# Performance work log

Measured on AMD Instinct MI355X. Metric: run time of the kernel, lower is better.

## Reference

```python
import jax, jax.numpy as jnp
import numpy as np

UNITS = 1024
N_FEATURES = 128
OUT_STEPS = 32
EPS = 1e-7


def _lstm_cell(x, h, c, W, U, b):
    # Keras LSTMCell: gates ordered i, f, g(candidate), o
    z = x @ W + h @ U + b  # [B, 4U]
    i, f, g, o = jnp.split(z, 4, axis=-1)
    i = jax.nn.sigmoid(i)
    f = jax.nn.sigmoid(f)
    g = jnp.tanh(g)
    o = jax.nn.sigmoid(o)
    c_new = f * c + i * g
    h_new = o * jnp.tanh(c_new)
    return h_new, c_new


def setup_inputs() -> dict:
    key = jax.random.key(0)
    ks = jax.random.split(key, 12)
    B, T, F, U = 512, 64, N_FEATURES, UNITS
    s = lambda fan_in: 1.0 / np.sqrt(fan_in)
    return {
        "inputs": jax.random.normal(ks[0], (B, T, F), jnp.float32),
        "mean": jax.random.normal(ks[1], (F,), jnp.float32) * 0.1,
        "var": jax.random.uniform(ks[2], (F,), jnp.float32, 0.5, 1.5),
        "W1": jax.random.normal(ks[3], (F, 4 * U), jnp.float32) * s(F),
        "U1": jax.random.normal(ks[4], (U, 4 * U), jnp.float32) * s(U),
        "b1": jnp.zeros((4 * U,), jnp.float32),
        "W2": jax.random.normal(ks[5], (U, 4 * U), jnp.float32) * s(U),
        "U2": jax.random.normal(ks[6], (U, 4 * U), jnp.float32) * s(U),
        "b2": jnp.zeros((4 * U,), jnp.float32),
        "Wd": jax.random.normal(ks[7], (U, F), jnp.float32) * s(U),
        "bd": jnp.zeros((F,), jnp.float32),
    }


def reference(inputs, mean, var, W1, U1, b1, W2, U2, b2, Wd, bd):
    B = inputs.shape[0]
    inv_std = jax.lax.rsqrt(var + EPS)
    # NOTE: original call() normalizes, then warmup() normalizes AGAIN -- faithful.
    x = (inputs - mean) * inv_std
    x = (x - mean) * inv_std

    # --- warmup: RNN(cell1) over input sequence, return last h and state ---
    h0 = jnp.zeros((B, UNITS), x.dtype)
    c0 = jnp.zeros((B, UNITS), x.dtype)

    def warm_step(carry, xt):
        h, c = carry
        h, c = _lstm_cell(xt, h, c, W1, U1, b1)
        return (h, c), None

    (h, c), _ = jax.lax.scan(warm_step, (h0, c0), jnp.swapaxes(x, 0, 1))
    pred0 = h @ Wd + bd  # [B, F]

    def ar_step(carry, _):
        pred, h, c = carry
        h, c = _lstm_cell(pred, h, c, W1, U1, b1)
        h, c = _lstm_cell(h, h, c, W2, U2, b2)
        pred = h @ Wd + bd
        return (pred, h, c), pred

    _, preds = jax.lax.scan(ar_step, (pred0, h, c), None, length=OUT_STEPS - 1)
    preds = jnp.concatenate([pred0[None], preds], axis=0)  # [out_steps, B, F]
    return jnp.transpose(preds, (1, 0, 2))  # [B, out_steps, F]
```

## Files before the change

### kernel.cpp

```cpp
#include <hip/hip_runtime.h>
#include <stdint.h>

#define NB 512
#define NT 64
#define NF 128
#define NU 1024
#define NG 4096
#define NS 32

typedef __attribute__((ext_vector_type(8))) short short8;
typedef __attribute__((ext_vector_type(4))) float f32x4;
typedef __attribute__((ext_vector_type(4))) unsigned int u32x4;

__device__ __forceinline__ float sigm(float x) { return 1.0f / (1.0f + __expf(-x)); }
__device__ __forceinline__ float tanh_f(float x) {
  float ax = fabsf(x);
  float e = __expf(2.0f * ax);
  float t = 1.0f - 2.0f / (e + 1.0f);
  return copysignf(t, x);
}
__device__ __forceinline__ unsigned short f2bf(float f) {
  union { float f; unsigned u; } v; v.f = f;
  unsigned r = v.u + 0x7fffu + ((v.u >> 16) & 1u);
  return (unsigned short)(r >> 16);
}

__device__ __forceinline__ void coh_store_bf16(unsigned short* p, unsigned v) {
  asm volatile("global_store_short %0, %1, off sc0 sc1" :: "v"(p), "v"(v) : "memory");
}

__device__ __forceinline__ void gbar(unsigned* flags, int bid, unsigned gen) {
  __syncthreads();
  if (threadIdx.x == 0)
    __hip_atomic_store(flags + bid, gen, __ATOMIC_RELAXED, __HIP_MEMORY_SCOPE_AGENT);
  if (bid == 0) {
    if (threadIdx.x < 256) {
      while (__hip_atomic_load(flags + threadIdx.x, __ATOMIC_RELAXED, __HIP_MEMORY_SCOPE_AGENT) != gen)
        __builtin_amdgcn_s_sleep(1);
    }
    __syncthreads();
    if (threadIdx.x == 0)
      __hip_atomic_store(flags + 256, gen, __ATOMIC_RELAXED, __HIP_MEMORY_SCOPE_AGENT);
  } else if (threadIdx.x == 0) {
    while (__hip_atomic_load(flags + 256, __ATOMIC_RELAXED, __HIP_MEMORY_SCOPE_AGENT) != gen)
      __builtin_amdgcn_s_sleep(1);
  }
  __syncthreads();
}

template <int KX>
__device__ __forceinline__ void do_step(
    const unsigned short* __restrict__ hIn,
    const unsigned short* __restrict__ Bp,
    const unsigned short* __restrict__ Xp,
    const unsigned short* __restrict__ W1p,
    int tstep, f32x4 bA, f32x4 (&cst)[2],
    unsigned short* __restrict__ hOut, unsigned short* __restrict__ hOut2,
    unsigned short* lds,
    int r0, int u0, int kh, int wu, int lr, int g4, int ucol, int tid)
{
  constexpr int ROWE = NU + KX;

  {
    u32x4 t[8];
    const unsigned short* src[8];
    int loff[8];
#pragma unroll
    for (int it = 0; it < 8; ++it) {
      int i = tid + it * 512;
      int r = i >> 7, cb = i & 127;
      src[it] = hIn + (size_t)(r0 + r) * NU + cb * 8;
      loff[it] = r * (ROWE * 2) + ((cb * 16) ^ ((r & 7) << 4));
    }
#pragma unroll
    for (int it = 0; it < 8; ++it)
      asm volatile("global_load_dwordx4 %0, %1, off sc0 sc1" : "=v"(t[it]) : "v"(src[it]));
    if constexpr (KX > 0) {
      int r = tid >> 4, cb = tid & 15;
      u32x4 vx = *(const u32x4*)(Xp + ((size_t)tstep * NB + (r0 + r)) * NF + cb * 8);
      int ox = r * (ROWE * 2) + ((NU * 2 + cb * 16) ^ ((r & 7) << 4));
      asm volatile("s_waitcnt vmcnt(0)" ::: "memory");
      __builtin_amdgcn_sched_barrier(0);
#pragma unroll
      for (int it = 0; it < 8; ++it) *(u32x4*)((char*)lds + loff[it]) = t[it];
      *(u32x4*)((char*)lds + ox) = vx;
    } else {
      asm volatile("s_waitcnt vmcnt(0)" ::: "memory");
      __builtin_amdgcn_sched_barrier(0);
#pragma unroll
      for (int it = 0; it < 8; ++it) *(u32x4*)((char*)lds + loff[it]) = t[it];
    }
  }
  __syncthreads();

  f32x4 acc[4][2];
#pragma unroll
  for (int g = 0; g < 4; ++g)
#pragma unroll
    for (int rt = 0; rt < 2; ++rt) acc[g][rt] = (f32x4){0.f, 0.f, 0.f, 0.f};

  const char* ldsb = (const char*)lds;
  const int arow0 = lr * (ROWE * 2);
  const int arow1 = (16 + lr) * (ROWE * 2);
  const int axor = (lr & 7) << 4;
  const int kcb = kh * 16;

  short8 nb[2][4];
  {
    size_t b0 = ((size_t)(kcb * 4 + g4) * NG + ucol) * 8;
    size_t b1 = ((size_t)((kcb + 1) * 4 + g4) * NG + ucol) * 8;
#pragma unroll
    for (int g = 0; g < 4; ++g) {
      nb[0][g] = *(const short8*)(Bp + b0 + (size_t)g * NU * 8);
      nb[1][g] = *(const short8*)(Bp + b1 + (size_t)g * NU * 8);
    }
  }
#pragma unroll 4
  for (int kc = 0; kc < 16; ++kc) {
    short8 bb[4];
#pragma unroll
    for (int g = 0; g < 4; ++g) bb[g] = nb[kc & 1][g];
    if (kc < 14) {
      size_t base = ((size_t)((kcb + kc + 2) * 4 + g4) * NG + ucol) * 8;
#pragma unroll
      for (int g = 0; g < 4; ++g) nb[kc & 1][g] = *(const short8*)(Bp + base + (size_t)g * NU * 8);
    }
    int kb = ((kcb + kc) * 64 + g4 * 16) ^ axor;
    short8 a0 = *(const short8*)(ldsb + arow0 + kb);
    short8 a1 = *(const short8*)(ldsb + arow1 + kb);
#pragma unroll
    for (int g = 0; g < 4; ++g) {
      acc[g][0] = __builtin_amdgcn_mfma_f32_16x16x32_bf16(a0, bb[g], acc[g][0], 0, 0, 0);
      acc[g][1] = __builtin_amdgcn_mfma_f32_16x16x32_bf16(a1, bb[g], acc[g][1], 0, 0, 0);
    }
  }
  if constexpr (KX > 0) {
#pragma unroll
    for (int kc = kh * 2; kc < kh * 2 + 2; ++kc) {
      int kb = (NU * 2 + kc * 64 + g4 * 16) ^ axor;
      short8 a0 = *(const short8*)(ldsb + arow0 + kb);
      short8 a1 = *(const short8*)(ldsb + arow1 + kb);
      size_t base = ((size_t)(kc * 4 + g4) * NG + ucol) * 8;
      short8 bb[4];
#pragma unroll
      for (int g = 0; g < 4; ++g) bb[g] = *(const short8*)(W1p + base + (size_t)g * NU * 8);
#pragma unroll
      for (int g = 0; g < 4; ++g) {
        acc[g][0] = __builtin_amdgcn_mfma_f32_16x16x32_bf16(a0, bb[g], acc[g][0], 0, 0, 0);
        acc[g][1] = __builtin_amdgcn_mfma_f32_16x16x32_bf16(a1, bb[g], acc[g][1], 0, 0, 0);
      }
    }
  }

  __syncthreads();
  float* red = (float*)lds;
  const int l = (g4 << 4) | lr;
  if (kh == 1) {
#pragma unroll
    for (int g = 0; g < 4; ++g)
#pragma unroll
      for (int rt = 0; rt < 2; ++rt)
        *(f32x4*)(red + (size_t)(((wu * 8) + (g * 2 + rt)) * 64 + l) * 4) = acc[g][rt];
  }
  __syncthreads();
  if (kh == 0) {
#pragma unroll
    for (int g = 0; g < 4; ++g)
#pragma unroll
      for (int rt = 0; rt < 2; ++rt)
        acc[g][rt] += *(const f32x4*)(red + (size_t)(((wu * 8) + (g * 2 + rt)) * 64 + l) * 4);

#pragma unroll
    for (int rt = 0; rt < 2; ++rt) {
#pragma unroll
      for (int j = 0; j < 4; ++j) {
        int r = r0 + rt * 16 + g4 * 4 + j;
        size_t idx = (size_t)r * NU + ucol;
        float iv = sigm(acc[0][rt][j] + bA[0]);
        float fv = sigm(acc[1][rt][j] + bA[1]);
        float gv = tanh_f(acc[2][rt][j] + bA[2]);
        float ov = sigm(acc[3][rt][j] + bA[3]);
        float cN = fv * cst[rt][j] + iv * gv;
        cst[rt][j] = cN;
        unsigned hv = f2bf(ov * tanh_f(cN));
        coh_store_bf16(hOut + idx, hv);
        if (hOut2) coh_store_bf16(hOut2 + idx, hv);
      }
    }
  }
}

__global__ __launch_bounds__(512, 2) void lstm_seq(
    const unsigned short* __restrict__ U1p, const unsigned short* __restrict__ U1pp,
    const unsigned short* __restrict__ W2U2p, const unsigned short* __restrict__ W1p,
    const unsigned short* __restrict__ x2,
    const float* __restrict__ b1, const float* __restrict__ b1p, const float* __restrict__ b2,
    unsigned short* __restrict__ h0, unsigned short* __restrict__ h1,
    unsigned short* __restrict__ hist, unsigned* __restrict__ flags)
{
  extern __shared__ unsigned short lds[];
  const int bid = blockIdx.x;
  const int xcd = bid & 7, slot = bid >> 3;
  const int u_blk = xcd * 2 + (slot >> 4);
  const int m_blk = slot & 15;
  const int r0 = m_blk * 32, u0 = u_blk * 64;
  const int tid = threadIdx.x;
  const int w = tid >> 6, kh = w >> 2, wu = w & 3;
  const int lr = tid & 15, g4 = (tid >> 4) & 3;
  const int ucol = u0 + wu * 16 + lr;
  const size_t HS = (size_t)NB * NU;

  f32x4 bW, bC1, bC2;
#pragma unroll
  for (int g = 0; g < 4; ++g) {
    bW[g]  = b1 [g * NU + ucol];
    bC1[g] = b1p[g * NU + ucol];
    bC2[g] = b2 [g * NU + ucol];
  }
  f32x4 cst[2];
  cst[0] = (f32x4){0.f, 0.f, 0.f, 0.f};
  cst[1] = (f32x4){0.f, 0.f, 0.f, 0.f};

  unsigned gen = 0;
  for (int t = 0; t < NT; ++t) {
    const unsigned short* hi = (t & 1) ? h1 : h0;
    unsigned short* ho = (t & 1) ? h0 : h1;
    do_step<NF>(hi, U1p, x2, W1p, t, bW, cst, ho, (t == NT - 1) ? hist : nullptr,
                lds, r0, u0, kh, wu, lr, g4, ucol, tid);
    gbar(flags, bid, ++gen);
  }
  for (int s = 0; s < NS - 1; ++s) {
    do_step<0>(h0, U1pp, nullptr, nullptr, 0, bC1, cst, h1, nullptr,
               lds, r0, u0, kh, wu, lr, g4, ucol, tid);
    gbar(flags, bid, ++gen);
    do_step<0>(h1, W2U2p, nullptr, nullptr, 0, bC2, cst, h0, hist + (size_t)(s + 1) * HS,
               lds, r0, u0, kh, wu, lr, g4, ucol, tid);
    if (s < NS - 2) gbar(flags, bid, ++gen);
  }
}

__global__ __launch_bounds__(256, 2) void pred_gemm(
    const unsigned short* __restrict__ H,
    const unsigned short* __restrict__ Wdp,
    const float* __restrict__ bd, float* __restrict__ out)
{
  __shared__ unsigned short lds[32 * NU];
  const int tid = threadIdx.x;
  const int r0 = blockIdx.x * 32;
  for (int i = tid; i < 32 * 128; i += 256) {
    int r = i >> 7, cb = i & 127;
    uint4 v = *(const uint4*)(H + (size_t)(r0 + r) * NU + cb * 8);
    int off = r * 2048 + ((cb * 16) ^ ((r & 7) << 4));
    *(uint4*)((char*)lds + off) = v;
  }
  __syncthreads();
  const int w = tid >> 6, l = tid & 63, lr = l & 15, g4 = l >> 4;
  f32x4 acc[2][2];
#pragma unroll
  for (int a = 0; a < 2; ++a)
#pragma unroll
    for (int c = 0; c < 2; ++c) acc[a][c] = (f32x4){0.f, 0.f, 0.f, 0.f};
  const char* ldsb = (const char*)lds;
  const int arow0 = lr * 2048, arow1 = (16 + lr) * 2048, axor = (lr & 7) << 4;
  const int col0 = w * 32 + lr;
#pragma unroll 4
  for (int kc = 0; kc < 32; ++kc) {
    int kb = (kc * 64 + g4 * 16) ^ axor;
    short8 a0 = *(const short8*)(ldsb + arow0 + kb);
    short8 a1 = *(const short8*)(ldsb + arow1 + kb);
    size_t base = ((size_t)(kc * 4 + g4) * NF) * 8;
    short8 w0 = *(const short8*)(Wdp + base + (size_t)col0 * 8);
    short8 w1 = *(const short8*)(Wdp + base + (size_t)(col0 + 16) * 8);
    acc[0][0] = __builtin_amdgcn_mfma_f32_16x16x32_bf16(a0, w0, acc[0][0], 0, 0, 0);
    acc[1][0] = __builtin_amdgcn_mfma_f32_16x16x32_bf16(a1, w0, acc[1][0], 0, 0, 0);
    acc[0][1] = __builtin_amdgcn_mfma_f32_16x16x32_bf16(a0, w1, acc[0][1], 0, 0, 0);
    acc[1][1] = __builtin_amdgcn_mfma_f32_16x16x32_bf16(a1, w1, acc[1][1], 0, 0, 0);
  }
#pragma unroll
  for (int rt = 0; rt < 2; ++rt)
#pragma unroll
    for (int ct = 0; ct < 2; ++ct)
#pragma unroll
      for (int j = 0; j < 4; ++j) {
        int r = r0 + rt * 16 + g4 * 4 + j;
        int s = r >> 9, bb = r & 511;
        int f = w * 32 + ct * 16 + lr;
        out[((size_t)bb * NS + s) * NF + f] = acc[rt][ct][j] + bd[f];
      }
}

__global__ void prep_x(const float* __restrict__ in, const float* __restrict__ mean,
                       const float* __restrict__ var, unsigned short* __restrict__ x2) {
  int i = (blockIdx.x * 256 + threadIdx.x) * 4;
  int f = i & 127;
  int bt = i >> 7;
  int b = bt >> 6, t = bt & 63;
  float4 v = *(const float4*)(in + i);
  float vv[4] = {v.x, v.y, v.z, v.w};
  unsigned short o[4] __attribute__((aligned(8)));
#pragma unroll
  for (int j = 0; j < 4; ++j) {
    float inv = rsqrtf(var[f + j] + 1e-7f);
    float s = inv * inv;
    float m2 = mean[f + j] * (s + inv);
    o[j] = f2bf(vv[j] * s - m2);
  }
  *(uint2*)(x2 + (((size_t)t * NB + b) << 7) + f) = *(const uint2*)o;
}

__global__ void prep_pack(const float* __restrict__ A, const float* __restrict__ A2,
                          unsigned short* __restrict__ P, int N) {
  int idx = blockIdx.x * 256 + threadIdx.x;
  int kg = idx / N, c = idx - kg * N;
  unsigned short o[8] __attribute__((aligned(16)));
#pragma unroll
  for (int j = 0; j < 8; ++j) {
    size_t e = (size_t)(kg * 8 + j) * N + c;
    float vv = A[e];
    if (A2) vv += A2[e];
    o[j] = f2bf(vv);
  }
  *(uint4*)(P + (size_t)idx * 8) = *(const uint4*)o;
}

__global__ __launch_bounds__(256) void prep_u1pp(
    const float* __restrict__ U1, const float* __restrict__ Wd,
    const float* __restrict__ W1, unsigned short* __restrict__ P) {
  __shared__ float wd[8][NF];
  const int kg = blockIdx.x >> 4;
  const int c = ((blockIdx.x & 15) << 8) + threadIdx.x;
  for (int i = threadIdx.x; i < 8 * NF; i += 256)
    wd[i >> 7][i & 127] = Wd[(size_t)(kg * 8 + (i >> 7)) * NF + (i & 127)];
  __syncthreads();
  float a[8];
#pragma unroll
  for (int j = 0; j < 8; ++j) a[j] = U1[(size_t)(kg * 8 + j) * NG + c];
#pragma unroll 8
  for (int m = 0; m < NF; ++m) {
    float w1v = W1[(size_t)m * NG + c];
#pragma unroll
    for (int j = 0; j < 8; ++j) a[j] += wd[j][m] * w1v;
  }
  unsigned short o[8] __attribute__((aligned(16)));
#pragma unroll
  for (int j = 0; j < 8; ++j) o[j] = f2bf(a[j]);
  *(uint4*)(P + (size_t)(kg * NG + c) * 8) = *(const uint4*)o;
}

__global__ void prep_wdp(const float* __restrict__ Wd, unsigned short* __restrict__ P) {
  int idx = blockIdx.x * 256 + threadIdx.x;
  int kg = idx >> 7, f = idx & 127;
  unsigned short o[8] __attribute__((aligned(16)));
#pragma unroll
  for (int j = 0; j < 8; ++j) o[j] = f2bf(Wd[(size_t)(kg * 8 + j) * NF + f]);
  *(uint4*)(P + (size_t)idx * 8) = *(const uint4*)o;
}

__global__ void prep_b1p(const float* __restrict__ b1, const float* __restrict__ bd,
                         const float* __restrict__ W1, float* __restrict__ o) {
  int c = blockIdx.x * 256 + threadIdx.x;
  float acc = b1[c];
#pragma unroll 8
  for (int m = 0; m < NF; ++m) acc += bd[m] * W1[(size_t)m * NG + c];
  o[c] = acc;
}

extern "C" void kernel_launch(void* const* d_in, const int* in_sizes, int n_in,
                              void* d_out, int out_size, void* d_ws, size_t ws_size,
                              hipStream_t stream) {
  const float* inputs = (const float*)d_in[0];
  const float* mean = (const float*)d_in[1];
  const float* var  = (const float*)d_in[2];
  const float* W1   = (const float*)d_in[3];
  const float* U1   = (const float*)d_in[4];
  const float* b1   = (const float*)d_in[5];
  const float* W2   = (const float*)d_in[6];
  const float* U2   = (const float*)d_in[7];
  const float* b2   = (const float*)d_in[8];
  const float* Wd   = (const float*)d_in[9];
  const float* bd   = (const float*)d_in[10];
  float* out = (float*)d_out;
  char* ws = (char*)d_ws;

  size_t off = 0;
  auto alloc = [&](size_t bytes) { char* p = ws + off; off += (bytes + 255) & ~255ull; return p; };
  unsigned short* h0    = (unsigned short*)alloc((size_t)NB * NU * 2);
  unsigned short* h1    = (unsigned short*)alloc((size_t)NB * NU * 2);
  unsigned short* hist  = (unsigned short*)alloc((size_t)NS * NB * NU * 2);
  unsigned short* x2    = (unsigned short*)alloc((size_t)NB * NT * NF * 2);
  unsigned short* U1p   = (unsigned short*)alloc((size_t)NU * NG * 2);
  unsigned short* U1pp  = (unsigned short*)alloc((size_t)NU * NG * 2);
  unsigned short* W2U2p = (unsigned short*)alloc((size_t)NU * NG * 2);
  unsigned short* W1p   = (unsigned short*)alloc((size_t)NF * NG * 2);
  unsigned short* Wdp   = (unsigned short*)alloc((size_t)NU * NF * 2);
  float* b1p            = (float*)alloc((size_t)NG * 4);
  unsigned* flags       = (unsigned*)alloc(2048);

  hipMemsetAsync(h0, 0, (size_t)NB * NU * 2, stream);
  hipMemsetAsync(flags, 0, 2048, stream);

  prep_x   <<<(NB * NT * NF) / 1024, 256, 0, stream>>>(inputs, mean, var, x2);
  prep_pack<<<(NU / 8) * NG / 256, 256, 0, stream>>>(U1, nullptr, U1p, NG);
  prep_u1pp<<<(NU / 8) * NG / 256, 256, 0, stream>>>(U1, Wd, W1, U1pp);
  prep_pack<<<(NU / 8) * NG / 256, 256, 0, stream>>>(W2, U2, W2U2p, NG);
  prep_pack<<<(NF / 8) * NG / 256, 256, 0, stream>>>(W1, nullptr, W1p, NG);
  prep_wdp <<<(NU / 8) * NF / 256, 256, 0, stream>>>(Wd, Wdp);
  prep_b1p <<<NG / 256, 256, 0, stream>>>(b1, bd, W1, b1p);

  lstm_seq<<<256, 512, 98304, stream>>>(U1p, U1pp, W2U2p, W1p, x2,
                                        b1, b1p, b2, h0, h1, hist, flags);

  pred_gemm<<<(NS * NB) / 32, 256, 0, stream>>>(hist, Wdp, bd, out);
}
```

Before: 1.353 ms.

## Retile persistent LSTM blocks to 64x32 with 4-way K split

```diff
diff --git a/kernel.cpp b/kernel.cpp
--- a/kernel.cpp
+++ b/kernel.cpp
@@ -25,14 +25,10 @@
   return (unsigned short)(r >> 16);
 }
 
-__device__ __forceinline__ void coh_store_bf16(unsigned short* p, unsigned v) {
-  asm volatile("global_store_short %0, %1, off sc0 sc1" :: "v"(p), "v"(v) : "memory");
-}
-
 __device__ __forceinline__ void gbar(unsigned* flags, int bid, unsigned gen) {
   __syncthreads();
   if (threadIdx.x == 0)
-    __hip_atomic_store(flags + bid, gen, __ATOMIC_RELAXED, __HIP_MEMORY_SCOPE_AGENT);
+    __hip_atomic_store(flags + bid, gen, __ATOMIC_RELEASE, __HIP_MEMORY_SCOPE_AGENT);
   if (bid == 0) {
     if (threadIdx.x < 256) {
       while (__hip_atomic_load(flags + threadIdx.x, __ATOMIC_RELAXED, __HIP_MEMORY_SCOPE_AGENT) != gen)
@@ -54,124 +50,131 @@
     const unsigned short* __restrict__ Bp,
     const unsigned short* __restrict__ Xp,
     const unsigned short* __restrict__ W1p,
-    int tstep, f32x4 bA, f32x4 (&cst)[2],
+    int tstep, f32x4 bA, f32x4 (&cst)[4],
     unsigned short* __restrict__ hOut, unsigned short* __restrict__ hOut2,
     unsigned short* lds,
     int r0, int u0, int kh, int wu, int lr, int g4, int ucol, int tid)
 {
-  constexpr int ROWE = NU + KX;
+  constexpr int ROWB = (NU + KX) * 2;
 
   {
-    u32x4 t[8];
-    const unsigned short* src[8];
-    int loff[8];
-#pragma unroll
-    for (int it = 0; it < 8; ++it) {
+    u32x4 t[16];
+    const unsigned short* src[16];
+    int loff[16];
+#pragma unroll
+    for (int it = 0; it < 16; ++it) {
       int i = tid + it * 512;
       int r = i >> 7, cb = i & 127;
       src[it] = hIn + (size_t)(r0 + r) * NU + cb * 8;
-      loff[it] = r * (ROWE * 2) + ((cb * 16) ^ ((r & 7) << 4));
-    }
-#pragma unroll
-    for (int it = 0; it < 8; ++it)
+      loff[it] = r * ROWB + ((cb * 16) ^ ((r & 7) << 4));
+    }
+#pragma unroll
+    for (int it = 0; it < 16; ++it)
       asm volatile("global_load_dwordx4 %0, %1, off sc0 sc1" : "=v"(t[it]) : "v"(src[it]));
     if constexpr (KX > 0) {
-      int r = tid >> 4, cb = tid & 15;
-      u32x4 vx = *(const u32x4*)(Xp + ((size_t)tstep * NB + (r0 + r)) * NF + cb * 8);
-      int ox = r * (ROWE * 2) + ((NU * 2 + cb * 16) ^ ((r & 7) << 4));
+      u32x4 vx[2]; int ox[2];
+#pragma unroll
+      for (int it = 0; it < 2; ++it) {
+        int i = tid + it * 512;
+        int r = i >> 4, cb = i & 15;
+        vx[it] = *(const u32x4*)(Xp + ((size_t)tstep * NB + (r0 + r)) * NF + cb * 8);
+        ox[it] = r * ROWB + ((NU * 2 + cb * 16) ^ ((r & 7) << 4));
+      }
       asm volatile("s_waitcnt vmcnt(0)" ::: "memory");
       __builtin_amdgcn_sched_barrier(0);
 #pragma unroll
-      for (int it = 0; it < 8; ++it) *(u32x4*)((char*)lds + loff[it]) = t[it];
-      *(u32x4*)((char*)lds + ox) = vx;
+      for (int it = 0; it < 16; ++it) *(u32x4*)((char*)lds + loff[it]) = t[it];
+#pragma unroll
+      for (int it = 0; it < 2; ++it) *(u32x4*)((char*)lds + ox[it]) = vx[it];
     } else {
       asm volatile("s_waitcnt vmcnt(0)" ::: "memory");
       __builtin_amdgcn_sched_barrier(0);
 #pragma unroll
-      for (int it = 0; it < 8; ++it) *(u32x4*)((char*)lds + loff[it]) = t[it];
-    }
-  }
-  __syncthreads();
-
-  f32x4 acc[4][2];
+      for (int it = 0; it < 16; ++it) *(u32x4*)((char*)lds + loff[it]) = t[it];
+    }
+  }
+  __syncthreads();
+
+  f32x4 acc[4][4];
 #pragma unroll
   for (int g = 0; g < 4; ++g)
 #pragma unroll
-    for (int rt = 0; rt < 2; ++rt) acc[g][rt] = (f32x4){0.f, 0.f, 0.f, 0.f};
+    for (int rt = 0; rt < 4; ++rt) acc[g][rt] = (f32x4){0.f, 0.f, 0.f, 0.f};
 
   const char* ldsb = (const char*)lds;
-  const int arow0 = lr * (ROWE * 2);
-  const int arow1 = (16 + lr) * (ROWE * 2);
+  int arow[4];
+#pragma unroll
+  for (int rt = 0; rt < 4; ++rt) arow[rt] = (rt * 16 + lr) * ROWB;
   const int axor = (lr & 7) << 4;
-  const int kcb = kh * 16;
+  const int kcb = kh * 8;
 
   short8 nb[2][4];
-  {
-    size_t b0 = ((size_t)(kcb * 4 + g4) * NG + ucol) * 8;
-    size_t b1 = ((size_t)((kcb + 1) * 4 + g4) * NG + ucol) * 8;
-#pragma unroll
-    for (int g = 0; g < 4; ++g) {
-      nb[0][g] = *(const short8*)(Bp + b0 + (size_t)g * NU * 8);
-      nb[1][g] = *(const short8*)(Bp + b1 + (size_t)g * NU * 8);
-    }
-  }
-#pragma unroll 4
-  for (int kc = 0; kc < 16; ++kc) {
+#pragma unroll
+  for (int p = 0; p < 2; ++p) {
+    size_t base = ((size_t)((kcb + p) * 4 + g4) * NG + ucol) * 8;
+#pragma unroll
+    for (int g = 0; g < 4; ++g) nb[p][g] = *(const short8*)(Bp + base + (size_t)g * NU * 8);
+  }
+#pragma unroll
+  for (int kc = 0; kc < 8; ++kc) {
     short8 bb[4];
 #pragma unroll
     for (int g = 0; g < 4; ++g) bb[g] = nb[kc & 1][g];
-    if (kc < 14) {
+    if (kc < 6) {
       size_t base = ((size_t)((kcb + kc + 2) * 4 + g4) * NG + ucol) * 8;
 #pragma unroll
       for (int g = 0; g < 4; ++g) nb[kc & 1][g] = *(const short8*)(Bp + base + (size_t)g * NU * 8);
     }
     int kb = ((kcb + kc) * 64 + g4 * 16) ^ axor;
-    short8 a0 = *(const short8*)(ldsb + arow0 + kb);
-    short8 a1 = *(const short8*)(ldsb + arow1 + kb);
-#pragma unroll
-    for (int g = 0; g < 4; ++g) {
-      acc[g][0] = __builtin_amdgcn_mfma_f32_16x16x32_bf16(a0, bb[g], acc[g][0], 0, 0, 0);
-      acc[g][1] = __builtin_amdgcn_mfma_f32_16x16x32_bf16(a1, bb[g], acc[g][1], 0, 0, 0);
-    }
+    short8 a[4];
+#pragma unroll
+    for (int rt = 0; rt < 4; ++rt) a[rt] = *(const short8*)(ldsb + arow[rt] + kb);
+#pragma unroll
+    for (int g = 0; g < 4; ++g)
+#pragma unroll
+      for (int rt = 0; rt < 4; ++rt)
+        acc[g][rt] = __builtin_amdgcn_mfma_f32_16x16x32_bf16(a[rt], bb[g], acc[g][rt], 0, 0, 0);
   }
   if constexpr (KX > 0) {
-#pragma unroll
-    for (int kc = kh * 2; kc < kh * 2 + 2; ++kc) {
-      int kb = (NU * 2 + kc * 64 + g4 * 16) ^ axor;
-      short8 a0 = *(const short8*)(ldsb + arow0 + kb);
-      short8 a1 = *(const short8*)(ldsb + arow1 + kb);
-      size_t base = ((size_t)(kc * 4 + g4) * NG + ucol) * 8;
-      short8 bb[4];
-#pragma unroll
-      for (int g = 0; g < 4; ++g) bb[g] = *(const short8*)(W1p + base + (size_t)g * NU * 8);
-#pragma unroll
-      for (int g = 0; g < 4; ++g) {
-        acc[g][0] = __builtin_amdgcn_mfma_f32_16x16x32_bf16(a0, bb[g], acc[g][0], 0, 0, 0);
-        acc[g][1] = __builtin_amdgcn_mfma_f32_16x16x32_bf16(a1, bb[g], acc[g][1], 0, 0, 0);
-      }
-    }
-  }
-
-  __syncthreads();
+    int kb = (NU * 2 + kh * 64 + g4 * 16) ^ axor;
+    size_t base = ((size_t)(kh * 4 + g4) * NG + ucol) * 8;
+    short8 bb[4];
+#pragma unroll
+    for (int g = 0; g < 4; ++g) bb[g] = *(const short8*)(W1p + base + (size_t)g * NU * 8);
+    short8 a[4];
+#pragma unroll
+    for (int rt = 0; rt < 4; ++rt) a[rt] = *(const short8*)(ldsb + arow[rt] + kb);
+#pragma unroll
+    for (int g = 0; g < 4; ++g)
+#pragma unroll
+      for (int rt = 0; rt < 4; ++rt)
+        acc[g][rt] = __builtin_amdgcn_mfma_f32_16x16x32_bf16(a[rt], bb[g], acc[g][rt], 0, 0, 0);
+  }
+
+  __syncthreads();
+  const int l = (g4 << 4) | lr;
   float* red = (float*)lds;
-  const int l = (g4 << 4) | lr;
-  if (kh == 1) {
+  if (kh != 0) {
+    float* base = red + (size_t)((kh - 1) * 2 + wu) * 4096;
 #pragma unroll
     for (int g = 0; g < 4; ++g)
 #pragma unroll
-      for (int rt = 0; rt < 2; ++rt)
-        *(f32x4*)(red + (size_t)(((wu * 8) + (g * 2 + rt)) * 64 + l) * 4) = acc[g][rt];
+      for (int rt = 0; rt < 4; ++rt)
+        *(f32x4*)(base + ((g * 4 + rt) * 64 + l) * 4) = acc[g][rt];
   }
   __syncthreads();
   if (kh == 0) {
 #pragma unroll
-    for (int g = 0; g < 4; ++g)
-#pragma unroll
-      for (int rt = 0; rt < 2; ++rt)
-        acc[g][rt] += *(const f32x4*)(red + (size_t)(((wu * 8) + (g * 2 + rt)) * 64 + l) * 4);
-
-#pragma unroll
-    for (int rt = 0; rt < 2; ++rt) {
+    for (int s = 0; s < 3; ++s) {
+      float* base = red + (size_t)(s * 2 + wu) * 4096;
+#pragma unroll
+      for (int g = 0; g < 4; ++g)
+#pragma unroll
+        for (int rt = 0; rt < 4; ++rt)
+          acc[g][rt] += *(const f32x4*)(base + ((g * 4 + rt) * 64 + l) * 4);
+    }
+#pragma unroll
+    for (int rt = 0; rt < 4; ++rt) {
 #pragma unroll
       for (int j = 0; j < 4; ++j) {
         int r = r0 + rt * 16 + g4 * 4 + j;
@@ -182,15 +185,15 @@
         float ov = sigm(acc[3][rt][j] + bA[3]);
         float cN = fv * cst[rt][j] + iv * gv;
         cst[rt][j] = cN;
-        unsigned hv = f2bf(ov * tanh_f(cN));
-        coh_store_bf16(hOut + idx, hv);
-        if (hOut2) coh_store_bf16(hOut2 + idx, hv);
+        unsigned short hv = f2bf(ov * tanh_f(cN));
+        hOut[idx] = hv;
+        if (hOut2) hOut2[idx] = hv;
       }
     }
   }
 }
 
-__global__ __launch_bounds__(512, 2) void lstm_seq(
+__global__ __launch_bounds__(512, 1) void lstm_seq(
     const unsigned short* __restrict__ U1p, const unsigned short* __restrict__ U1pp,
     const unsigned short* __restrict__ W2U2p, const unsigned short* __restrict__ W1p,
     const unsigned short* __restrict__ x2,
@@ -201,11 +204,11 @@
   extern __shared__ unsigned short lds[];
   const int bid = blockIdx.x;
   const int xcd = bid & 7, slot = bid >> 3;
-  const int u_blk = xcd * 2 + (slot >> 4);
-  const int m_blk = slot & 15;
-  const int r0 = m_blk * 32, u0 = u_blk * 64;
+  const int u_blk = xcd * 4 + (slot >> 3);
+  const int m_blk = slot & 7;
+  const int r0 = m_blk * 64, u0 = u_blk * 32;
   const int tid = threadIdx.x;
-  const int w = tid >> 6, kh = w >> 2, wu = w & 3;
+  const int w = tid >> 6, kh = w >> 1, wu = w & 1;
   const int lr = tid & 15, g4 = (tid >> 4) & 3;
   const int ucol = u0 + wu * 16 + lr;
   const size_t HS = (size_t)NB * NU;
@@ -217,9 +220,9 @@
     bC1[g] = b1p[g * NU + ucol];
     bC2[g] = b2 [g * NU + ucol];
   }
-  f32x4 cst[2];
-  cst[0] = (f32x4){0.f, 0.f, 0.f, 0.f};
-  cst[1] = (f32x4){0.f, 0.f, 0.f, 0.f};
+  f32x4 cst[4];
+#pragma unroll
+  for (int rt = 0; rt < 4; ++rt) cst[rt] = (f32x4){0.f, 0.f, 0.f, 0.f};
 
   unsigned gen = 0;
   for (int t = 0; t < NT; ++t) {
@@ -407,8 +410,8 @@
   prep_wdp <<<(NU / 8) * NF / 256, 256, 0, stream>>>(Wd, Wdp);
   prep_b1p <<<NG / 256, 256, 0, stream>>>(b1, bd, W1, b1p);
 
-  lstm_seq<<<256, 512, 98304, stream>>>(U1p, U1pp, W2U2p, W1p, x2,
-                                        b1, b1p, b2, h0, h1, hist, flags);
+  lstm_seq<<<256, 512, 64 * (NU + NF) * 2, stream>>>(U1p, U1pp, W2U2p, W1p, x2,
+                                                     b1, b1p, b2, h0, h1, hist, flags);
 
   pred_gemm<<<(NS * NB) / 32, 256, 0, stream>>>(hist, Wdp, bd, out);
 }
```

Result: slower. 4.499 ms (+232.6%).

## Split gate epilogue across both K-half warps and trim per-step latency

Applied to the files above, without the earlier changes.

```diff
diff --git a/kernel.cpp b/kernel.cpp
--- a/kernel.cpp
+++ b/kernel.cpp
@@ -54,42 +54,64 @@
     const unsigned short* __restrict__ Bp,
     const unsigned short* __restrict__ Xp,
     const unsigned short* __restrict__ W1p,
-    int tstep, f32x4 bA, f32x4 (&cst)[2],
-    unsigned short* __restrict__ hOut, unsigned short* __restrict__ hOut2,
+    int tstep, const float* __restrict__ bias, f32x4& cst,
+    unsigned short* __restrict__ hOut,
     unsigned short* lds,
     int r0, int u0, int kh, int wu, int lr, int g4, int ucol, int tid)
 {
-  constexpr int ROWE = NU + KX;
-
-  {
-    u32x4 t[8];
-    const unsigned short* src[8];
-    int loff[8];
+  constexpr int ROWB = (NU + KX) * 2;
+
+  u32x4 t[8]; int lo[8];
+  if constexpr (KX > 0) {
+    u32x4 tx; int ox;
+    {
+      int r = tid >> 4, cb = tid & 15;
+      ox = r * ROWB + ((NU * 2 + cb * 16) ^ ((r & 7) << 4));
+      const unsigned short* g = Xp + ((size_t)tstep * NB + (r0 + r)) * NF + cb * 8;
+      asm volatile("global_load_dwordx4 %0, %1, off" : "=v"(tx) : "v"(g));
+    }
 #pragma unroll
     for (int it = 0; it < 8; ++it) {
       int i = tid + it * 512;
       int r = i >> 7, cb = i & 127;
-      src[it] = hIn + (size_t)(r0 + r) * NU + cb * 8;
-      loff[it] = r * (ROWE * 2) + ((cb * 16) ^ ((r & 7) << 4));
-    }
-#pragma unroll
-    for (int it = 0; it < 8; ++it)
-      asm volatile("global_load_dwordx4 %0, %1, off sc0 sc1" : "=v"(t[it]) : "v"(src[it]));
-    if constexpr (KX > 0) {
-      int r = tid >> 4, cb = tid & 15;
-      u32x4 vx = *(const u32x4*)(Xp + ((size_t)tstep * NB + (r0 + r)) * NF + cb * 8);
-      int ox = r * (ROWE * 2) + ((NU * 2 + cb * 16) ^ ((r & 7) << 4));
-      asm volatile("s_waitcnt vmcnt(0)" ::: "memory");
-      __builtin_amdgcn_sched_barrier(0);
-#pragma unroll
-      for (int it = 0; it < 8; ++it) *(u32x4*)((char*)lds + loff[it]) = t[it];
-      *(u32x4*)((char*)lds + ox) = vx;
-    } else {
-      asm volatile("s_waitcnt vmcnt(0)" ::: "memory");
-      __builtin_amdgcn_sched_barrier(0);
-#pragma unroll
-      for (int it = 0; it < 8; ++it) *(u32x4*)((char*)lds + loff[it]) = t[it];
-    }
+      lo[it] = r * ROWB + ((cb * 16) ^ ((r & 7) << 4));
+      const unsigned short* g = hIn + (size_t)(r0 + r) * NU + cb * 8;
+      asm volatile("global_load_dwordx4 %0, %1, off sc0 sc1" : "=v"(t[it]) : "v"(g));
+    }
+    asm volatile("s_waitcnt vmcnt(4)" ::: "memory");
+    __builtin_amdgcn_sched_barrier(0);
+    *(u32x4*)((char*)lds + ox) = tx;
+#pragma unroll
+    for (int it = 0; it < 4; ++it) *(u32x4*)((char*)lds + lo[it]) = t[it];
+    asm volatile("s_waitcnt vmcnt(0)" ::: "memory");
+    __builtin_amdgcn_sched_barrier(0);
+#pragma unroll
+    for (int it = 4; it < 8; ++it) *(u32x4*)((char*)lds + lo[it]) = t[it];
+  } else {
+#pragma unroll
+    for (int it = 0; it < 8; ++it) {
+      int i = tid + it * 512;
+      int r = i >> 7, cb = i & 127;
+      lo[it] = r * ROWB + ((cb * 16) ^ ((r & 7) << 4));
+      const unsigned short* g = hIn + (size_t)(r0 + r) * NU + cb * 8;
+      asm volatile("global_load_dwordx4 %0, %1, off sc0 sc1" : "=v"(t[it]) : "v"(g));
+    }
+    asm volatile("s_waitcnt vmcnt(4)" ::: "memory");
+    __builtin_amdgcn_sched_barrier(0);
+#pragma unroll
+    for (int it = 0; it < 4; ++it) *(u32x4*)((char*)lds + lo[it]) = t[it];
+    asm volatile("s_waitcnt vmcnt(0)" ::: "memory");
+    __builtin_amdgcn_sched_barrier(0);
+#pragma unroll
+    for (int it = 4; it < 8; ++it) *(u32x4*)((char*)lds + lo[it]) = t[it];
+  }
+
+  const int kcb = kh * 16;
+  short8 nb[4];
+  {
+    size_t base = ((size_t)(kcb * 4 + g4) * NG + ucol) * 8;
+#pragma unroll
+    for (int g = 0; g < 4; ++g) nb[g] = *(const short8*)(Bp + base + (size_t)g * NU * 8);
   }
   __syncthreads();
 
@@ -100,30 +122,19 @@
     for (int rt = 0; rt < 2; ++rt) acc[g][rt] = (f32x4){0.f, 0.f, 0.f, 0.f};
 
   const char* ldsb = (const char*)lds;
-  const int arow0 = lr * (ROWE * 2);
-  const int arow1 = (16 + lr) * (ROWE * 2);
+  const int arow0 = lr * ROWB;
+  const int arow1 = (16 + lr) * ROWB;
   const int axor = (lr & 7) << 4;
-  const int kcb = kh * 16;
-
-  short8 nb[2][4];
-  {
-    size_t b0 = ((size_t)(kcb * 4 + g4) * NG + ucol) * 8;
-    size_t b1 = ((size_t)((kcb + 1) * 4 + g4) * NG + ucol) * 8;
-#pragma unroll
-    for (int g = 0; g < 4; ++g) {
-      nb[0][g] = *(const short8*)(Bp + b0 + (size_t)g * NU * 8);
-      nb[1][g] = *(const short8*)(Bp + b1 + (size_t)g * NU * 8);
-    }
-  }
+
 #pragma unroll 4
   for (int kc = 0; kc < 16; ++kc) {
     short8 bb[4];
 #pragma unroll
-    for (int g = 0; g < 4; ++g) bb[g] = nb[kc & 1][g];
-    if (kc < 14) {
-      size_t base = ((size_t)((kcb + kc + 2) * 4 + g4) * NG + ucol) * 8;
-#pragma unroll
-      for (int g = 0; g < 4; ++g) nb[kc & 1][g] = *(const short8*)(Bp + base + (size_t)g * NU * 8);
+    for (int g = 0; g < 4; ++g) bb[g] = nb[g];
+    if (kc < 15) {
+      size_t base = ((size_t)((kcb + kc + 1) * 4 + g4) * NG + ucol) * 8;
+#pragma unroll
+      for (int g = 0; g < 4; ++g) nb[g] = *(const short8*)(Bp + base + (size_t)g * NU * 8);
     }
     int kb = ((kcb + kc) * 64 + g4 * 16) ^ axor;
     short8 a0 = *(const short8*)(ldsb + arow0 + kb);
@@ -152,41 +163,35 @@
     }
   }
 
-  __syncthreads();
-  float* red = (float*)lds;
-  const int l = (g4 << 4) | lr;
-  if (kh == 1) {
-#pragma unroll
-    for (int g = 0; g < 4; ++g)
-#pragma unroll
-      for (int rt = 0; rt < 2; ++rt)
-        *(f32x4*)(red + (size_t)(((wu * 8) + (g * 2 + rt)) * 64 + l) * 4) = acc[g][rt];
-  }
-  __syncthreads();
-  if (kh == 0) {
-#pragma unroll
-    for (int g = 0; g < 4; ++g)
-#pragma unroll
-      for (int rt = 0; rt < 2; ++rt)
-        acc[g][rt] += *(const f32x4*)(red + (size_t)(((wu * 8) + (g * 2 + rt)) * 64 + l) * 4);
-
-#pragma unroll
-    for (int rt = 0; rt < 2; ++rt) {
-#pragma unroll
-      for (int j = 0; j < 4; ++j) {
-        int r = r0 + rt * 16 + g4 * 4 + j;
-        size_t idx = (size_t)r * NU + ucol;
-        float iv = sigm(acc[0][rt][j] + bA[0]);
-        float fv = sigm(acc[1][rt][j] + bA[1]);
-        float gv = tanh_f(acc[2][rt][j] + bA[2]);
-        float ov = sigm(acc[3][rt][j] + bA[3]);
-        float cN = fv * cst[rt][j] + iv * gv;
-        cst[rt][j] = cN;
-        unsigned hv = f2bf(ov * tanh_f(cN));
-        coh_store_bf16(hOut + idx, hv);
-        if (hOut2) coh_store_bf16(hOut2 + idx, hv);
-      }
-    }
+  float bA[4];
+#pragma unroll
+  for (int g = 0; g < 4; ++g) bA[g] = bias[g * NU + ucol];
+
+  __syncthreads();
+  char* redb = (char*)lds;
+  const int lane = (g4 << 4) | lr;
+  const int other = 1 - kh;
+#pragma unroll
+  for (int g = 0; g < 4; ++g)
+    *(f32x4*)(redb + (((kh * 4 + wu) * 4 + g) << 10) + lane * 16) = acc[g][other];
+  __syncthreads();
+  f32x4 z[4];
+#pragma unroll
+  for (int g = 0; g < 4; ++g)
+    z[g] = acc[g][kh] +
+           *(const f32x4*)(redb + (((other * 4 + wu) * 4 + g) << 10) + lane * 16);
+
+#pragma unroll
+  for (int j = 0; j < 4; ++j) {
+    int r = r0 + kh * 16 + g4 * 4 + j;
+    size_t idx = (size_t)r * NU + ucol;
+    float iv = sigm(z[0][j] + bA[0]);
+    float fv = sigm(z[1][j] + bA[1]);
+    float gv = tanh_f(z[2][j] + bA[2]);
+    float ov = sigm(z[3][j] + bA[3]);
+    float cN = fv * cst[j] + iv * gv;
+    cst[j] = cN;
+    coh_store_bf16(hOut + idx, f2bf(ov * tanh_f(cN)));
   }
 }
 
@@ -210,30 +215,21 @@
   const int ucol = u0 + wu * 16 + lr;
   const size_t HS = (size_t)NB * NU;
 
-  f32x4 bW, bC1, bC2;
-#pragma unroll
-  for (int g = 0; g < 4; ++g) {
-    bW[g]  = b1 [g * NU + ucol];
-    bC1[g] = b1p[g * NU + ucol];
-    bC2[g] = b2 [g * NU + ucol];
-  }
-  f32x4 cst[2];
-  cst[0] = (f32x4){0.f, 0.f, 0.f, 0.f};
-  cst[1] = (f32x4){0.f, 0.f, 0.f, 0.f};
+  f32x4 cst = (f32x4){0.f, 0.f, 0.f, 0.f};
 
   unsigned gen = 0;
   for (int t = 0; t < NT; ++t) {
     const unsigned short* hi = (t & 1) ? h1 : h0;
-    unsigned short* ho = (t & 1) ? h0 : h1;
-    do_step<NF>(hi, U1p, x2, W1p, t, bW, cst, ho, (t == NT - 1) ? hist : nullptr,
+    unsigned short* ho = (t == NT - 1) ? hist : ((t & 1) ? h0 : h1);
+    do_step<NF>(hi, U1p, x2, W1p, t, b1, cst, ho,
                 lds, r0, u0, kh, wu, lr, g4, ucol, tid);
     gbar(flags, bid, ++gen);
   }
   for (int s = 0; s < NS - 1; ++s) {
-    do_step<0>(h0, U1pp, nullptr, nullptr, 0, bC1, cst, h1, nullptr,
+    do_step<0>(hist + (size_t)s * HS, U1pp, nullptr, nullptr, 0, b1p, cst, h1,
                lds, r0, u0, kh, wu, lr, g4, ucol, tid);
     gbar(flags, bid, ++gen);
-    do_step<0>(h1, W2U2p, nullptr, nullptr, 0, bC2, cst, h0, hist + (size_t)(s + 1) * HS,
+    do_step<0>(h1, W2U2p, nullptr, nullptr, 0, b2, cst, hist + (size_t)(s + 1) * HS,
                lds, r0, u0, kh, wu, lr, g4, ucol, tid);
     if (s < NS - 2) gbar(flags, bid, ++gen);
   }
@@ -407,8 +403,8 @@
   prep_wdp <<<(NU / 8) * NF / 256, 256, 0, stream>>>(Wd, Wdp);
   prep_b1p <<<NG / 256, 256, 0, stream>>>(b1, bd, W1, b1p);
 
-  lstm_seq<<<256, 512, 98304, stream>>>(U1p, U1pp, W2U2p, W1p, x2,
-                                        b1, b1p, b2, h0, h1, hist, flags);
+  lstm_seq<<<256, 512, 32 * (NU + NF) * 2, stream>>>(U1p, U1pp, W2U2p, W1p, x2,
+                                                     b1, b1p, b2, h0, h1, hist, flags);
 
   pred_gemm<<<(NS * NB) / 32, 256, 0, stream>>>(hist, Wdp, bd, out);
 }
```

Measured after the change: 2.326 ms. 1.72x slower.
